# Optimization experiments

Measured on AMD Instinct MI355X. Metric: run time of the kernel, lower is better.

## Reference

```python
import jax, jax.numpy as jnp
import numpy as np

N_SUBJECTS = 16
N_LABELS = 8
DENS_TEMP = 0.1  # args.ProtoSim_dens_temp


def setup_inputs() -> dict:
    key = jax.random.key(0)
    k1, k2, k3 = jax.random.split(key, 3)
    B, C, D = 16384, 2, 1024
    X_data = jax.random.normal(k1, (B, C, D), dtype=jnp.float32)
    subject = jax.random.randint(k2, (B,), 0, N_SUBJECTS, dtype=jnp.int64) if jax.config.jax_enable_x64 else jax.random.randint(k2, (B,), 0, N_SUBJECTS).astype(jnp.int32)
    labels = jax.random.randint(k3, (B,), 0, N_LABELS).astype(subject.dtype)
    return {"X_data": X_data, "subject": subject, "labels": labels}


def reference(X_data, subject, labels):
    B, C, D = X_data.shape
    K = N_SUBJECTS * N_LABELS  # all (subject,label) groups assumed present
    # contrast_feature = cat(unbind(X_data, 1), 0) -> [B*C, D]
    feat = X_data.swapaxes(0, 1).reshape(B * C, D)
    sub2 = jnp.tile(subject, C)          # cat((subject, subject))
    lab2 = jnp.tile(labels, C)
    # torch.unique sorts -> group g = subject * N_LABELS + label matches loop order
    gid = sub2 * N_LABELS + lab2
    counts = jax.ops.segment_sum(jnp.ones((B * C,), feat.dtype), gid, num_segments=K)  # (K,)
    centroid = jax.ops.segment_sum(feat, gid, num_segments=K) / counts[:, None]       # (K, D)
    # per-row euclidean distance to own group centroid (torch.cdist to 1 point)
    dist = jnp.linalg.norm(feat - centroid[gid], axis=1)                               # (B*C,)
    mean_sqrt = jax.ops.segment_sum(jnp.sqrt(dist), gid, num_segments=K) / counts
    density = mean_sqrt / jnp.log(counts + 10.0)
    density = jnp.where(counts <= 1.0, density.max(), density)
    density = jnp.clip(density, jnp.quantile(density, 0.1), jnp.quantile(density, 0.9))
    density = DENS_TEMP * density / density.mean()                                     # (K,)
    # masks: positives = same label, different subject
    g_sub = jnp.arange(K) // N_LABELS
    g_lab = jnp.arange(K) % N_LABELS
    subj_mask = (sub2[:, None] != g_sub[None, :]).astype(feat.dtype)  # (B*C, K)
    lab_mask = (lab2[:, None] == g_lab[None, :]).astype(feat.dtype)
    mask = subj_mask * lab_mask
    # every row has N_SUBJECTS-1 positives (all groups present), so no row filtering
    sim = (feat @ centroid.T) / density[None, :]                                        # (B*C, K)
    sim = sim - sim.max(axis=1, keepdims=True)
    pos = sim * mask
    logp = jax.nn.log_softmax(pos, axis=1)
    row_loss = -(mask * logp).sum(axis=1) / mask.sum(axis=1)  # soft-target CE / #pos
    return row_loss.reshape(C, B).mean()
```

## Files before the change

### kernel.cpp

```cpp
#include <hip/hip_runtime.h>
#include <hip/hip_bf16.h>
#include <math.h>

#define NSUB 16
#define NLAB 8
#define KG 128
#define BN 16384
#define DD 1024

typedef float v4f __attribute__((ext_vector_type(4)));
typedef short short8v __attribute__((ext_vector_type(8)));
typedef unsigned short ushort4v __attribute__((ext_vector_type(4)));

static __device__ __forceinline__ short f2bf(float f) {
    unsigned u = __builtin_bit_cast(unsigned, f);
    unsigned r = (u + 0x7fffu + ((u >> 16) & 1u)) >> 16;
    return (short)r;
}

static __device__ __forceinline__ float bf2f(unsigned short u) {
    unsigned v = ((unsigned)u) << 16;
    return __builtin_bit_cast(float, v);
}

static __device__ __forceinline__ unsigned packbf2(float x, float y) {
    union { __hip_bfloat162 h; unsigned u; } c;
    c.h = __float22bfloat162_rn(float2{x, y});
    return c.u;
}

__global__ __launch_bounds__(1024) void k0_gid(const int* __restrict__ subject,
                                               const int* __restrict__ labels,
                                               int* __restrict__ gid, int* __restrict__ hist) {
    __shared__ int h[KG];
    int t = threadIdx.x;
    if (t < KG) h[t] = 0;
    __syncthreads();
    int b = blockIdx.x * 1024 + t;
    int g = subject[b] * NLAB + labels[b];
    gid[b] = g;
    atomicAdd(&h[g], 1);
    __syncthreads();
    if (t < KG) hist[blockIdx.x * KG + t] = h[t];
}

__global__ __launch_bounds__(1024) void k0c_scatter(const int* __restrict__ gid,
                                                    const int* __restrict__ hist,
                                                    int* __restrict__ cnt,
                                                    int* __restrict__ rowlist) {
    __shared__ int tots[KG], base0[KG], lcur[KG];
    int t = threadIdx.x, bi = blockIdx.x;
    if (t < KG) {
        int tot = 0, pre = 0;
#pragma unroll
        for (int j = 0; j < 16; ++j) {
            int v = hist[j * KG + t];
            tot += v;
            if (j < bi) pre += v;
        }
        tots[t] = tot;
        base0[t] = pre;
        lcur[t] = 0;
        if (bi == 0) cnt[t] = tot;
    }
    __syncthreads();
    if (t < KG) {
        int o = 0;
        for (int j = 0; j < t; ++j) o += tots[j];
        base0[t] += o;
    }
    __syncthreads();
    int b = bi * 1024 + t;
    int g = gid[b];
    rowlist[base0[g] + atomicAdd(&lcur[g], 1)] = b;
}

__global__ __launch_bounds__(256) void k1_centroid(const float* __restrict__ X,
                                                   const int* __restrict__ rowlist,
                                                   const int* __restrict__ cnt,
                                                   unsigned short* __restrict__ Btil,
                                                   float* __restrict__ cnormPart) {
    int g = blockIdx.x >> 1;
    int half = blockIdx.x & 1;
    int t = threadIdx.x, lane = t & 63, w = t >> 6;
    int d = half * 512 + t * 2;
    int kc = d >> 5, q = (d >> 3) & 3, jj = d & 7;
    int base_t = kc * 512 + q * 128 + jj;
    __shared__ int rows[512];
    __shared__ int sh_no[2];
    __shared__ float wsum[4];
    if (w == 0) {
        int v = 0;
        if (lane < g) v += cnt[lane];
        if (lane + 64 < g) v += cnt[lane + 64];
#pragma unroll
        for (int x = 32; x; x >>= 1) v += __shfl_xor(v, x, 64);
        if (lane == 0) { sh_no[0] = v; sh_no[1] = cnt[g]; }
    }
    __syncthreads();
    int o = sh_no[0], n = min(sh_no[1], 512);
    for (int i = t; i < n; i += 256) rows[i] = rowlist[o + i];
    __syncthreads();
    float ax = 0.f, ay = 0.f;
    int i = 0;
    for (; i + 16 <= n; i += 16) {
        float2 v[32];
#pragma unroll
        for (int u = 0; u < 16; ++u) {
            size_t base = (size_t)rows[i + u] * 2048 + d;
            v[2 * u] = *(const float2*)(X + base);
            v[2 * u + 1] = *(const float2*)(X + base + 1024);
        }
#pragma unroll
        for (int u = 0; u < 32; ++u) { ax += v[u].x; ay += v[u].y; }
    }
    for (; i < n; ++i) {
        size_t base = (size_t)rows[i] * 2048 + d;
        float2 v0 = *(const float2*)(X + base);
        float2 v1 = *(const float2*)(X + base + 1024);
        ax += v0.x + v1.x; ay += v0.y + v1.y;
    }
    float inv = 1.f / (2.f * (float)n);
    float cx = ax * inv, cy = ay * inv;
    int gt = g >> 4, mc = g & 15;
    *(unsigned*)(Btil + (size_t)gt * 16384 + mc * 8 + base_t) = packbf2(cx, cy);
    float s = cx * cx + cy * cy;
#pragma unroll
    for (int x = 32; x; x >>= 1) s += __shfl_xor(s, x, 64);
    if (lane == 0) wsum[w] = s;
    __syncthreads();
    if (t == 0) cnormPart[half * KG + g] = wsum[0] + wsum[1] + wsum[2] + wsum[3];
}

__global__ __launch_bounds__(256) void k2_tile(const float* __restrict__ X,
                                               unsigned short* __restrict__ Atil) {
    __shared__ unsigned lds[8192];
    int t = threadIdx.x, lane = t & 63, w = t >> 6;
    int rt = blockIdx.x;
#pragma unroll
    for (int p = 0; p < 4; ++p) {
        int m = w * 4 + p;
        int r = rt * 16 + m;
        const float* xp = X + (size_t)(r & (BN - 1)) * 2048 + (size_t)(r >> 14) * 1024;
        unsigned swz = (unsigned)((m & 7) << 2);
        unsigned mbase = (unsigned)m * 512;
#pragma unroll
        for (int j = 0; j < 4; ++j) {
            int d0 = j * 256 + lane * 4;
            float4 v = *(const float4*)(xp + d0);
            unsigned wi = mbase + (((unsigned)(d0 >> 1)) ^ swz);
            lds[wi] = packbf2(v.x, v.y);
            lds[wi + 1] = packbf2(v.z, v.w);
        }
    }
    __syncthreads();
    size_t gbase = (size_t)rt * 16384;
#pragma unroll
    for (int p = 0; p < 8; ++p) {
        int wo = p * 1024 + t * 4;
        int kc = wo >> 8;
        int q = (wo >> 6) & 3;
        int m = (wo >> 2) & 15;
        unsigned wi = (unsigned)m * 512 +
                      (((unsigned)(kc * 16 + q * 4)) ^ (unsigned)((m & 7) << 2));
        uint4 val = *(const uint4*)&lds[wi];
        *(uint4*)(Atil + gbase + (size_t)wo * 2) = val;
    }
}

__global__ __launch_bounds__(256) void k5a_dot(const unsigned short* __restrict__ Atil,
                                               const unsigned short* __restrict__ Btil,
                                               const int* __restrict__ gid,
                                               const float* __restrict__ cnormPart,
                                               unsigned short* __restrict__ Dotb,
                                               float* __restrict__ sqsPart) {
    __shared__ float h[KG];
    __shared__ float cnormS[KG];
    int t = threadIdx.x, lane = t & 63;
    if (t < KG) {
        h[t] = 0.f;
        cnormS[t] = cnormPart[t] + cnormPart[KG + t];
    }
    __syncthreads();
    int gw = blockIdx.x * 4 + (t >> 6);
    int row0 = gw * 32;
    int m = lane & 15, q = lane >> 4;
    const unsigned short* a0 = Atil + (size_t)(gw * 2) * 16384 + lane * 8;
    const unsigned short* a1 = a0 + 16384;
    const unsigned short* bb = Btil + lane * 8;

    v4f acc[2][8];
#pragma unroll
    for (int i = 0; i < 2; ++i)
#pragma unroll
        for (int j = 0; j < 8; ++j) acc[i][j] = (v4f){0.f, 0.f, 0.f, 0.f};

    short8v A0[4], A1[4], Bf[4][8];
#pragma unroll
    for (int p = 0; p < 4; ++p) {
        A0[p] = *(const short8v*)(a0 + p * 512);
        A1[p] = *(const short8v*)(a1 + p * 512);
#pragma unroll
        for (int gt = 0; gt < 8; ++gt)
            Bf[p][gt] = *(const short8v*)(bb + (size_t)gt * 16384 + p * 512);
    }
    float s0 = 0.f, s1 = 0.f;
#pragma unroll
    for (int kc = 0; kc < 32; ++kc) {
        const int cur = kc & 3;
        short8v nA0, nA1, nB[8];
        if (kc + 4 < 32) {
            nA0 = *(const short8v*)(a0 + (kc + 4) * 512);
            nA1 = *(const short8v*)(a1 + (kc + 4) * 512);
#pragma unroll
            for (int gt = 0; gt < 8; ++gt)
                nB[gt] = *(const short8v*)(bb + (size_t)gt * 16384 + (kc + 4) * 512);
        }
#pragma unroll
        for (int gt = 0; gt < 8; ++gt) {
            acc[0][gt] = __builtin_amdgcn_mfma_f32_16x16x32_bf16(A0[cur], Bf[cur][gt], acc[0][gt], 0, 0, 0);
            acc[1][gt] = __builtin_amdgcn_mfma_f32_16x16x32_bf16(A1[cur], Bf[cur][gt], acc[1][gt], 0, 0, 0);
        }
        {
            union { short8v s; unsigned u[4]; } ua, ub;
            ua.s = A0[cur]; ub.s = A1[cur];
#pragma unroll
            for (int r = 0; r < 4; ++r) {
                float l0 = __builtin_bit_cast(float, ua.u[r] << 16);
                float h0 = __builtin_bit_cast(float, ua.u[r] & 0xffff0000u);
                s0 = fmaf(l0, l0, s0); s0 = fmaf(h0, h0, s0);
                float l1 = __builtin_bit_cast(float, ub.u[r] << 16);
                float h1 = __builtin_bit_cast(float, ub.u[r] & 0xffff0000u);
                s1 = fmaf(l1, l1, s1); s1 = fmaf(h1, h1, s1);
            }
        }
        if (kc + 4 < 32) {
            A0[cur] = nA0; A1[cur] = nA1;
#pragma unroll
            for (int gt = 0; gt < 8; ++gt) Bf[cur][gt] = nB[gt];
        }
    }

    s0 += __shfl_xor(s0, 16, 64); s0 += __shfl_xor(s0, 32, 64);
    s1 += __shfl_xor(s1, 16, 64); s1 += __shfl_xor(s1, 32, 64);

    int rowblk = row0 >> 6, rlo = row0 & 32;
#pragma unroll
    for (int tile = 0; tile < 2; ++tile)
#pragma unroll
        for (int reg = 0; reg < 4; ++reg) {
            int rr = rlo + tile * 16 + q * 4 + reg;
            int row = (rowblk << 6) + rr;
            int b = row & (BN - 1);
            int g = gid[b];
            float own = 0.f;
#pragma unroll
            for (int gt = 0; gt < 8; ++gt) {
                float v = acc[tile][gt][reg];
                size_t idx = (((size_t)rowblk * 32 + gt * 4 + (m >> 2)) * 64 + rr) * 4 + (m & 3);
                Dotb[idx] = (unsigned short)f2bf(v);
                if ((g >> 4) == gt) own = v;
            }
            float rn = __shfl(tile ? s1 : s0, q * 4 + reg, 64);
            if ((g & 15) == m) {
                float d2 = fmaxf(rn - 2.f * own + cnormS[g], 0.f);
                atomicAdd(&h[g], sqrtf(sqrtf(d2)));
            }
        }
    __syncthreads();
    if (t < KG) sqsPart[(size_t)blockIdx.x * KG + t] = h[t];
}

__global__ __launch_bounds__(128) void k5b_loss(const unsigned short* __restrict__ Dotb,
                                                const int* __restrict__ gid,
                                                const float* __restrict__ sqsPart,
                                                const int* __restrict__ cnt,
                                                float* __restrict__ out) {
    __shared__ float tmp[KG], d1s[KG], qv[4];
    __shared__ float recipDen[KG];
    __shared__ float wsum[2];
    int t = threadIdx.x;
    float cntf = 0.f, d0v = 0.f, v = 0.f;
    if (t < KG) {
        float ss = 0.f;
        for (int j = 0; j < 256; j += 4)
            ss += sqsPart[(size_t)j * KG + t] + sqsPart[(size_t)(j + 1) * KG + t] +
                  sqsPart[(size_t)(j + 2) * KG + t] + sqsPart[(size_t)(j + 3) * KG + t];
        cntf = 2.f * (float)cnt[t];
        d0v = (ss / cntf) / logf(cntf + 10.f);
        tmp[t] = d0v;
    }
    __syncthreads();
    if (t < KG) {
        float dmax = -INFINITY;
        for (int j = 0; j < KG; ++j) dmax = fmaxf(dmax, tmp[j]);
        v = (cntf <= 1.f) ? dmax : d0v;
        d1s[t] = v;
    }
    __syncthreads();
    if (t < KG) {
        int less = 0, eq = 0;
        for (int j = 0; j < KG; ++j) {
            float u = d1s[j];
            less += (u < v) ? 1 : 0;
            eq += (u == v) ? 1 : 0;
        }
        const int ppos[4] = {12, 13, 114, 115};
        for (int qq = 0; qq < 4; ++qq)
            if (less <= ppos[qq] && ppos[qq] < less + eq) qv[qq] = v;
    }
    __syncthreads();
    if (t < KG) {
        float q10 = 0.3f * qv[0] + 0.7f * qv[1];
        float q90 = 0.7f * qv[2] + 0.3f * qv[3];
        tmp[t] = fminf(fmaxf(v, q10), q90);
    }
    __syncthreads();
    if (t < KG) {
        float sum = 0.f;
        for (int j = 0; j < KG; ++j) sum += tmp[j];
        float mean = sum / (float)KG;
        recipDen[t] = mean / (0.1f * tmp[t]);
    }
    __syncthreads();
    int row = blockIdx.x * 128 + t;
    int b = row & (BN - 1);
    int g = gid[b];
    int s = g >> 3, l = g & 7;
    int lane = t & 63, w = t >> 6;
    size_t rowblk = (size_t)(row >> 6);
    const ushort4v* dp = (const ushort4v*)Dotb;
    float mx = -INFINITY;
    float psave[16];
#pragma unroll
    for (int c = 0; c < 16; ++c) {
        size_t i0 = (rowblk * 32 + c * 2) * 64 + lane;
        ushort4v dv0 = dp[i0];
        ushort4v dv1 = dp[i0 + 64];
        const float* rv = &recipDen[c * 8];
        float x[8];
#pragma unroll
        for (int j = 0; j < 4; ++j) x[j] = bf2f((unsigned short)dv0[j]) * rv[j];
#pragma unroll
        for (int j = 0; j < 4; ++j) x[4 + j] = bf2f((unsigned short)dv1[j]) * rv[4 + j];
#pragma unroll
        for (int j = 0; j < 8; ++j) mx = fmaxf(mx, x[j]);
        float sel = x[0];
#pragma unroll
        for (int j = 1; j < 8; ++j) sel = (j == l) ? x[j] : sel;
        psave[c] = sel;
    }
    float S = 0.f, P = 0.f;
#pragma unroll
    for (int j = 0; j < 16; ++j) {
        float pv = psave[j] - mx;
        float e = expf(pv);
        bool use = (j != s);
        S += use ? e : 0.f;
        P += use ? pv : 0.f;
    }
    float ll = logf(113.f + S) - P * (1.f / 15.f);
#pragma unroll
    for (int x2 = 32; x2; x2 >>= 1) ll += __shfl_xor(ll, x2, 64);
    if (lane == 0) wsum[w] = ll;
    __syncthreads();
    if (t == 0) atomicAdd(out, (wsum[0] + wsum[1]) * (1.f / 32768.f));
}

extern "C" void kernel_launch(void* const* d_in, const int* in_sizes, int n_in,
                              void* d_out, int out_size, void* d_ws, size_t ws_size,
                              hipStream_t stream) {
    const float* X = (const float*)d_in[0];
    const int* subject = (const int*)d_in[1];
    const int* labels = (const int*)d_in[2];
    float* out = (float*)d_out;
    char* w = (char*)d_ws;
    int* gid = (int*)(w + 0);
    int* hist = (int*)(w + 65536);
    int* cnt = (int*)(w + 73728);
    float* cnormPart = (float*)(w + 74240);
    int* rowlist = (int*)(w + 131072);
    float* sqsPart = (float*)(w + 262144);
    unsigned short* Btil = (unsigned short*)(w + 524288);
    unsigned short* Atil = (unsigned short*)(w + 2097152);
    unsigned short* Dotb = (unsigned short*)(w + 100663296);

    (void)hipMemsetAsync(out, 0, sizeof(float), stream);

    k0_gid<<<16, 1024, 0, stream>>>(subject, labels, gid, hist);
    k0c_scatter<<<16, 1024, 0, stream>>>(gid, hist, cnt, rowlist);
    k1_centroid<<<KG * 2, 256, 0, stream>>>(X, rowlist, cnt, Btil, cnormPart);
    k2_tile<<<2048, 256, 0, stream>>>(X, Atil);
    k5a_dot<<<256, 256, 0, stream>>>(Atil, Btil, gid, cnormPart, Dotb, sqsPart);
    k5b_loss<<<256, 128, 0, stream>>>(Dotb, gid, sqsPart, cnt, out);
}
```

Baseline: 261.3 us.

## Halve per-wave rows in dot kernel and widen centroid loads to float4

The dot kernel now gives each wave one 16-row tile instead of two and launches twice as many blocks, with a 2-deep prefetch instead of 4-deep. This lowers register pressure and raises occupancy and parallelism, but B fragments are reloaded twice as often. The loss kernel is updated to sum the doubled number of partial histograms. The centroid kernel splits threads by channel and uses float4 loads with a shared-memory reduction, replacing float2 pairs.

```diff
diff --git a/kernel.cpp b/kernel.cpp
--- a/kernel.cpp
+++ b/kernel.cpp
@@ -83,12 +83,11 @@
     int g = blockIdx.x >> 1;
     int half = blockIdx.x & 1;
     int t = threadIdx.x, lane = t & 63, w = t >> 6;
-    int d = half * 512 + t * 2;
-    int kc = d >> 5, q = (d >> 3) & 3, jj = d & 7;
-    int base_t = kc * 512 + q * 128 + jj;
+    int c = t >> 7, td = t & 127;
     __shared__ int rows[512];
     __shared__ int sh_no[2];
-    __shared__ float wsum[4];
+    __shared__ float acc4[256][4];
+    __shared__ float wsum[2];
     if (w == 0) {
         int v = 0;
         if (lane < g) v += cnt[lane];
@@ -101,35 +100,46 @@
     int o = sh_no[0], n = min(sh_no[1], 512);
     for (int i = t; i < n; i += 256) rows[i] = rowlist[o + i];
     __syncthreads();
-    float ax = 0.f, ay = 0.f;
+    size_t coff = (size_t)c * 1024 + half * 512 + td * 4;
+    float4 s4 = make_float4(0.f, 0.f, 0.f, 0.f);
     int i = 0;
-    for (; i + 16 <= n; i += 16) {
-        float2 v[32];
-#pragma unroll
-        for (int u = 0; u < 16; ++u) {
-            size_t base = (size_t)rows[i + u] * 2048 + d;
-            v[2 * u] = *(const float2*)(X + base);
-            v[2 * u + 1] = *(const float2*)(X + base + 1024);
-        }
-#pragma unroll
-        for (int u = 0; u < 32; ++u) { ax += v[u].x; ay += v[u].y; }
+    for (; i + 8 <= n; i += 8) {
+        float4 v[8];
+#pragma unroll
+        for (int u = 0; u < 8; ++u)
+            v[u] = *(const float4*)(X + (size_t)rows[i + u] * 2048 + coff);
+#pragma unroll
+        for (int u = 0; u < 8; ++u) {
+            s4.x += v[u].x; s4.y += v[u].y; s4.z += v[u].z; s4.w += v[u].w;
+        }
     }
     for (; i < n; ++i) {
-        size_t base = (size_t)rows[i] * 2048 + d;
-        float2 v0 = *(const float2*)(X + base);
-        float2 v1 = *(const float2*)(X + base + 1024);
-        ax += v0.x + v1.x; ay += v0.y + v1.y;
-    }
-    float inv = 1.f / (2.f * (float)n);
-    float cx = ax * inv, cy = ay * inv;
-    int gt = g >> 4, mc = g & 15;
-    *(unsigned*)(Btil + (size_t)gt * 16384 + mc * 8 + base_t) = packbf2(cx, cy);
-    float s = cx * cx + cy * cy;
+        float4 v = *(const float4*)(X + (size_t)rows[i] * 2048 + coff);
+        s4.x += v.x; s4.y += v.y; s4.z += v.z; s4.w += v.w;
+    }
+    acc4[t][0] = s4.x; acc4[t][1] = s4.y; acc4[t][2] = s4.z; acc4[t][3] = s4.w;
+    __syncthreads();
+    float s = 0.f;
+    if (t < 128) {
+        float inv = 1.f / (2.f * (float)n);
+        float cx[4];
+#pragma unroll
+        for (int j = 0; j < 4; ++j) {
+            cx[j] = (acc4[t][j] + acc4[t + 128][j]) * inv;
+            s += cx[j] * cx[j];
+        }
+        int dd = half * 512 + t * 4;
+        int base_t = (dd >> 5) * 512 + ((dd >> 3) & 3) * 128 + (g & 15) * 8 + (dd & 7);
+        uint2 st;
+        st.x = packbf2(cx[0], cx[1]);
+        st.y = packbf2(cx[2], cx[3]);
+        *(uint2*)(Btil + (size_t)(g >> 4) * 16384 + base_t) = st;
+    }
 #pragma unroll
     for (int x = 32; x; x >>= 1) s += __shfl_xor(s, x, 64);
-    if (lane == 0) wsum[w] = s;
-    __syncthreads();
-    if (t == 0) cnormPart[half * KG + g] = wsum[0] + wsum[1] + wsum[2] + wsum[3];
+    if (lane == 0) wsum[w & 1] = (w < 2) ? s : 0.f;
+    __syncthreads();
+    if (t == 0) cnormPart[half * KG + g] = wsum[0] + wsum[1];
 }
 
 __global__ __launch_bounds__(256) void k2_tile(const float* __restrict__ X,
@@ -176,97 +186,83 @@
                                                float* __restrict__ sqsPart) {
     __shared__ float h[KG];
     __shared__ float cnormS[KG];
-    int t = threadIdx.x, lane = t & 63;
+    int t = threadIdx.x, lane = t & 63, w = t >> 6;
     if (t < KG) {
         h[t] = 0.f;
         cnormS[t] = cnormPart[t] + cnormPart[KG + t];
     }
     __syncthreads();
-    int gw = blockIdx.x * 4 + (t >> 6);
-    int row0 = gw * 32;
+    int rt = blockIdx.x * 4 + w;
     int m = lane & 15, q = lane >> 4;
-    const unsigned short* a0 = Atil + (size_t)(gw * 2) * 16384 + lane * 8;
-    const unsigned short* a1 = a0 + 16384;
-    const unsigned short* bb = Btil + lane * 8;
-
-    v4f acc[2][8];
-#pragma unroll
-    for (int i = 0; i < 2; ++i)
-#pragma unroll
-        for (int j = 0; j < 8; ++j) acc[i][j] = (v4f){0.f, 0.f, 0.f, 0.f};
-
-    short8v A0[4], A1[4], Bf[4][8];
-#pragma unroll
-    for (int p = 0; p < 4; ++p) {
-        A0[p] = *(const short8v*)(a0 + p * 512);
-        A1[p] = *(const short8v*)(a1 + p * 512);
+    const unsigned short* ap = Atil + (size_t)rt * 16384 + lane * 8;
+    const unsigned short* bp = Btil + lane * 8;
+
+    v4f acc[8];
+#pragma unroll
+    for (int j = 0; j < 8; ++j) acc[j] = (v4f){0.f, 0.f, 0.f, 0.f};
+
+    short8v Af[2], Bf[2][8];
+#pragma unroll
+    for (int p = 0; p < 2; ++p) {
+        Af[p] = *(const short8v*)(ap + p * 512);
 #pragma unroll
         for (int gt = 0; gt < 8; ++gt)
-            Bf[p][gt] = *(const short8v*)(bb + (size_t)gt * 16384 + p * 512);
-    }
-    float s0 = 0.f, s1 = 0.f;
+            Bf[p][gt] = *(const short8v*)(bp + (size_t)gt * 16384 + p * 512);
+    }
+    float s0 = 0.f;
 #pragma unroll
     for (int kc = 0; kc < 32; ++kc) {
-        const int cur = kc & 3;
-        short8v nA0, nA1, nB[8];
-        if (kc + 4 < 32) {
-            nA0 = *(const short8v*)(a0 + (kc + 4) * 512);
-            nA1 = *(const short8v*)(a1 + (kc + 4) * 512);
+        const int cur = kc & 1;
+        short8v nA, nB[8];
+        if (kc + 2 < 32) {
+            nA = *(const short8v*)(ap + (kc + 2) * 512);
 #pragma unroll
             for (int gt = 0; gt < 8; ++gt)
-                nB[gt] = *(const short8v*)(bb + (size_t)gt * 16384 + (kc + 4) * 512);
-        }
-#pragma unroll
-        for (int gt = 0; gt < 8; ++gt) {
-            acc[0][gt] = __builtin_amdgcn_mfma_f32_16x16x32_bf16(A0[cur], Bf[cur][gt], acc[0][gt], 0, 0, 0);
-            acc[1][gt] = __builtin_amdgcn_mfma_f32_16x16x32_bf16(A1[cur], Bf[cur][gt], acc[1][gt], 0, 0, 0);
-        }
+                nB[gt] = *(const short8v*)(bp + (size_t)gt * 16384 + (kc + 2) * 512);
+        }
+#pragma unroll
+        for (int gt = 0; gt < 8; ++gt)
+            acc[gt] = __builtin_amdgcn_mfma_f32_16x16x32_bf16(Af[cur], Bf[cur][gt], acc[gt], 0, 0, 0);
         {
-            union { short8v s; unsigned u[4]; } ua, ub;
-            ua.s = A0[cur]; ub.s = A1[cur];
+            union { short8v s; unsigned u[4]; } ua;
+            ua.s = Af[cur];
 #pragma unroll
             for (int r = 0; r < 4; ++r) {
                 float l0 = __builtin_bit_cast(float, ua.u[r] << 16);
                 float h0 = __builtin_bit_cast(float, ua.u[r] & 0xffff0000u);
                 s0 = fmaf(l0, l0, s0); s0 = fmaf(h0, h0, s0);
-                float l1 = __builtin_bit_cast(float, ub.u[r] << 16);
-                float h1 = __builtin_bit_cast(float, ub.u[r] & 0xffff0000u);
-                s1 = fmaf(l1, l1, s1); s1 = fmaf(h1, h1, s1);
             }
         }
-        if (kc + 4 < 32) {
-            A0[cur] = nA0; A1[cur] = nA1;
+        if (kc + 2 < 32) {
+            Af[cur] = nA;
 #pragma unroll
             for (int gt = 0; gt < 8; ++gt) Bf[cur][gt] = nB[gt];
         }
     }
 
     s0 += __shfl_xor(s0, 16, 64); s0 += __shfl_xor(s0, 32, 64);
-    s1 += __shfl_xor(s1, 16, 64); s1 += __shfl_xor(s1, 32, 64);
-
-    int rowblk = row0 >> 6, rlo = row0 & 32;
-#pragma unroll
-    for (int tile = 0; tile < 2; ++tile)
-#pragma unroll
-        for (int reg = 0; reg < 4; ++reg) {
-            int rr = rlo + tile * 16 + q * 4 + reg;
-            int row = (rowblk << 6) + rr;
-            int b = row & (BN - 1);
-            int g = gid[b];
-            float own = 0.f;
-#pragma unroll
-            for (int gt = 0; gt < 8; ++gt) {
-                float v = acc[tile][gt][reg];
-                size_t idx = (((size_t)rowblk * 32 + gt * 4 + (m >> 2)) * 64 + rr) * 4 + (m & 3);
-                Dotb[idx] = (unsigned short)f2bf(v);
-                if ((g >> 4) == gt) own = v;
-            }
-            float rn = __shfl(tile ? s1 : s0, q * 4 + reg, 64);
-            if ((g & 15) == m) {
-                float d2 = fmaxf(rn - 2.f * own + cnormS[g], 0.f);
-                atomicAdd(&h[g], sqrtf(sqrtf(d2)));
-            }
-        }
+
+    int bid = blockIdx.x;
+#pragma unroll
+    for (int reg = 0; reg < 4; ++reg) {
+        int rr = w * 16 + q * 4 + reg;
+        int row = bid * 64 + rr;
+        int b = row & (BN - 1);
+        int g = gid[b];
+        float own = 0.f;
+#pragma unroll
+        for (int gt = 0; gt < 8; ++gt) {
+            float v = acc[gt][reg];
+            size_t idx = (((size_t)bid * 32 + gt * 4 + (m >> 2)) * 64 + rr) * 4 + (m & 3);
+            Dotb[idx] = (unsigned short)f2bf(v);
+            if ((g >> 4) == gt) own = v;
+        }
+        float rn = __shfl(s0, q * 4 + reg, 64);
+        if ((g & 15) == m) {
+            float d2 = fmaxf(rn - 2.f * own + cnormS[g], 0.f);
+            atomicAdd(&h[g], sqrtf(sqrtf(d2)));
+        }
+    }
     __syncthreads();
     if (t < KG) sqsPart[(size_t)blockIdx.x * KG + t] = h[t];
 }
@@ -283,7 +279,7 @@
     float cntf = 0.f, d0v = 0.f, v = 0.f;
     if (t < KG) {
         float ss = 0.f;
-        for (int j = 0; j < 256; j += 4)
+        for (int j = 0; j < 512; j += 4)
             ss += sqsPart[(size_t)j * KG + t] + sqsPart[(size_t)(j + 1) * KG + t] +
                   sqsPart[(size_t)(j + 2) * KG + t] + sqsPart[(size_t)(j + 3) * KG + t];
         cntf = 2.f * (float)cnt[t];
@@ -391,6 +387,6 @@
     k0c_scatter<<<16, 1024, 0, stream>>>(gid, hist, cnt, rowlist);
     k1_centroid<<<KG * 2, 256, 0, stream>>>(X, rowlist, cnt, Btil, cnormPart);
     k2_tile<<<2048, 256, 0, stream>>>(X, Atil);
-    k5a_dot<<<256, 256, 0, stream>>>(Atil, Btil, gid, cnormPart, Dotb, sqsPart);
+    k5a_dot<<<512, 256, 0, stream>>>(Atil, Btil, gid, cnormPart, Dotb, sqsPart);
     k5b_loss<<<256, 128, 0, stream>>>(Dotb, gid, sqsPart, cnt, out);
 }
```

After: 267.3 us. 2.3% more time.
